# Optimization experiments

Measured on AMD Instinct MI355X. Metric: run time of the kernel, lower is better.

The kernel has to match this reference:

```python
import jax, jax.numpy as jnp
import numpy as np

RELU_NEG_SLOPE = 0.2

def _gat_layer(x, W, a, src, dst, num_nodes, concat):
    # x: [N, Din]; W: [H, Din, F]; a: [H, 2F]; src/dst: [E]
    H, _, F = W.shape
    proj = jnp.einsum('nd,hdf->nhf', x, W)              # [N, H, F]
    a_self, a_nb = a[:, :F], a[:, F:]                   # [H, F] each
    alpha_self = jnp.einsum('nhf,hf->nh', proj, a_self) # [N, H]
    alpha_nb = jnp.einsum('nhf,hf->nh', proj, a_nb)     # [N, H]
    # edge score: a . [proj_dst || proj_src], dst = center node i, src = neighbor j
    e = jax.nn.leaky_relu(alpha_self[dst] + alpha_nb[src], RELU_NEG_SLOPE)  # [E, H]
    e_max = jax.ops.segment_max(e, dst, num_segments=num_nodes)
    e_exp = jnp.exp(e - e_max[dst])
    denom = jax.ops.segment_sum(e_exp, dst, num_segments=num_nodes)
    w = e_exp / denom[dst]                              # [E, H] softmax per dst node
    msg = proj[src] * w[:, :, None]                     # [E, H, F]
    out = jax.ops.segment_sum(msg, dst, num_segments=num_nodes)  # [N, H, F]
    if concat:
        return out.reshape(num_nodes, H * F)
    return out.mean(axis=1)


def setup_inputs() -> dict:
    key = jax.random.key(0)
    k1, k2, k3, k4, k5, k6 = jax.random.split(key, 6)
    N, Din, F1, H1 = 10000, 128, 64, 8
    Dmid = H1 * F1  # 512
    F2, H2 = 64, 1
    x = jax.random.normal(k1, (N, Din), dtype=jnp.float32)
    edges = jax.random.randint(k2, (2, 80000), 0, N, dtype=jnp.int64)
    W1 = jax.random.normal(k3, (H1, Din, F1), dtype=jnp.float32) / np.sqrt(Din)
    a1 = jax.random.normal(k4, (H1, 2 * F1), dtype=jnp.float32) / np.sqrt(2 * F1)
    W2 = jax.random.normal(k5, (H2, Dmid, F2), dtype=jnp.float32) / np.sqrt(Dmid)
    a2 = jax.random.normal(k6, (H2, 2 * F2), dtype=jnp.float32) / np.sqrt(2 * F2)
    return {"x": x, "edges": edges, "W1": W1, "a1": a1, "W2": W2, "a2": a2}


def reference(x, edges, W1, a1, W2, a2):
    N = x.shape[0]
    loops = jnp.arange(N, dtype=edges.dtype)
    # undirected graph + self loops (Graph.neighborhood adds both directions and self)
    src = jnp.concatenate([edges[0], edges[1], loops])
    dst = jnp.concatenate([edges[1], edges[0], loops])
    h = _gat_layer(x, W1, a1, src, dst, N, concat=True)   # [N, 512]
    h = jax.nn.elu(h)
    out = _gat_layer(h, W2, a2, src, dst, N, concat=False)  # [N, 64]
    return out
```

## Files before the change

### kernel.cpp

```cpp
#include <hip/hip_runtime.h>
#include <hip/hip_fp16.h>

#define RELU_NEG_SLOPE 0.2f

typedef _Float16 half8 __attribute__((ext_vector_type(8)));
typedef float f32x4 __attribute__((ext_vector_type(4)));

__device__ __forceinline__ float leaky(float e) {
    return (e > 0.f) ? e : RELU_NEG_SLOPE * e;
}

__device__ __forceinline__ float elu1(float x) {
    return (x > 0.f) ? x : (__expf(x) - 1.f);
}

#define MAXN 16384
#define MAXPAD 16384

__device__ __align__(256) int            g_cnt[MAXN];
__device__ __align__(256) unsigned short g_ell[MAXN * 64];
__device__ __align__(256) __half         g_proj1p[(size_t)4 * MAXPAD * 128];
__device__ __align__(256) __half         g_hbufh[(size_t)MAXPAD * 512];
__device__ __align__(256) __half         g_W2t[64 * 512];
__device__ __align__(256) __half         g_proj2h[MAXN * 64];
__device__ __align__(256) float          g_as1[MAXN * 8];
__device__ __align__(256) float          g_an1[MAXN * 8];
__device__ __align__(256) float          g_as2[MAXN];
__device__ __align__(256) float          g_an2[MAXN];

__global__ __launch_bounds__(256) void k1_scatter_gemm1(
    const int* __restrict__ edges, int E0,
    const float* __restrict__ W2, int t2, int nscat,
    const float4* __restrict__ x4, const float* __restrict__ W1,
    const float* __restrict__ a1, int N, int slabN) {
    __shared__ __half Bs[64 * 132];
    if (blockIdx.x < nscat) {
        int i = blockIdx.x * 256 + threadIdx.x;
        if (i < 2 * E0) {
            int s = edges[i];
            int d = (i < E0) ? edges[E0 + i] : edges[i - E0];
            int pos = atomicAdd(&g_cnt[d], 1);
            g_ell[(d << 6) + pos] = (unsigned short)s;
        } else if (i < 2 * E0 + t2) {
            int j = i - 2 * E0;
            int f = j & 63;
            int d = j >> 6;
            g_W2t[f * 512 + d] = __float2half(W2[j]);
        }
        return;
    }
    int bid2 = blockIdx.x - nscat;
    const int h = bid2 & 7;
    const int by = bid2 >> 3;

    {
        const float4* W1h = (const float4*)W1 + h * 2048;
        int t = threadIdx.x;
#pragma unroll
        for (int r = 0; r < 8; r++) {
            int j4 = t + r * 256;
            float4 w = W1h[j4];
            int f = (j4 << 2) & 63;
            int d = j4 >> 4;
            Bs[(f + 0) * 132 + d] = __float2half(w.x);
            Bs[(f + 1) * 132 + d] = __float2half(w.y);
            Bs[(f + 2) * 132 + d] = __float2half(w.z);
            Bs[(f + 3) * 132 + d] = __float2half(w.w);
        }
    }
    __syncthreads();

    const int lane = threadIdx.x & 63;
    const int wave = threadIdx.x >> 6;
    const int q = lane >> 4;
    const int l15 = lane & 15;
    const int mrow = by * 64 + wave * 16;

    int arow = mrow + l15;
    if (arow >= N) arow = N - 1;
    const float4* Ar = x4 + (size_t)arow * 32;

    f32x4 acc[4] = {{0.f, 0.f, 0.f, 0.f}, {0.f, 0.f, 0.f, 0.f},
                    {0.f, 0.f, 0.f, 0.f}, {0.f, 0.f, 0.f, 0.f}};
#pragma unroll
    for (int ks = 0; ks < 4; ks++) {
        float4 a0 = Ar[ks * 8 + q * 2];
        float4 a1v = Ar[ks * 8 + q * 2 + 1];
        half8 av;
        av[0] = (_Float16)a0.x; av[1] = (_Float16)a0.y;
        av[2] = (_Float16)a0.z; av[3] = (_Float16)a0.w;
        av[4] = (_Float16)a1v.x; av[5] = (_Float16)a1v.y;
        av[6] = (_Float16)a1v.z; av[7] = (_Float16)a1v.w;
#pragma unroll
        for (int t = 0; t < 4; t++) {
            half8 bv = *(const half8*)(Bs + (t * 16 + l15) * 132 + q * 8 + ks * 32);
            acc[t] = __builtin_amdgcn_mfma_f32_16x16x32_f16(av, bv, acc[t], 0, 0, 0);
        }
    }

    __half* Cs = g_proj1p + (size_t)(h >> 1) * slabN + (h & 1) * 64;
    float asc[4], anc[4];
#pragma unroll
    for (int t = 0; t < 4; t++) {
        asc[t] = a1[h * 128 + t * 16 + l15];
        anc[t] = a1[h * 128 + 64 + t * 16 + l15];
    }
#pragma unroll
    for (int r = 0; r < 4; r++) {
        int mg = mrow + q * 4 + r;
        float ps = 0.f, pn = 0.f;
#pragma unroll
        for (int t = 0; t < 4; t++) {
            float v = acc[t][r];
            ps += v * asc[t];
            pn += v * anc[t];
            if (mg < N)
                Cs[(size_t)mg * 128 + t * 16 + l15] = __float2half(v);
        }
#pragma unroll
        for (int m = 8; m >= 1; m >>= 1) {
            ps += __shfl_xor(ps, m, 64);
            pn += __shfl_xor(pn, m, 64);
        }
        if (l15 == 0 && mg < N) {
            g_as1[mg * 8 + h] = ps;
            g_an1[mg * 8 + h] = pn;
        }
    }
}

__global__ __launch_bounds__(256) void agg_h8_sliced(int N, int slabN) {
    int bid = blockIdx.x;
    int hp = bid & 3;
    int rem = bid >> 2;
    int d = rem * 4 + (threadIdx.x >> 6);
    int lane = threadIdx.x & 63;
    if (d >= N) return;
    const int sub = lane >> 3;
    const int inner = lane & 7;
    const int hh = inner >> 2;
    const int h = hp * 2 + hh;
    const int c16 = (inner & 3) * 16;

    int deg = g_cnt[d];
    const unsigned short* row = g_ell + (d << 6);
    float asd = g_as1[d * 8 + h];
    const __half* slab = g_proj1p + (size_t)hp * slabN;

    float acc[16];
#pragma unroll
    for (int i = 0; i < 16; i++) acc[i] = 0.f;
    float den = 0.f;
    if (sub == 0) {
        float e = __expf(leaky(asd + g_an1[d * 8 + h]));
        const __half* p = slab + (size_t)d * 128 + hh * 64 + c16;
        half8 v0 = *(const half8*)p;
        half8 v1 = *(const half8*)(p + 8);
        den = e;
#pragma unroll
        for (int i = 0; i < 8; i++) {
            acc[i] = e * (float)v0[i];
            acc[8 + i] = e * (float)v1[i];
        }
    }
    for (int j0 = 0; j0 < deg; j0 += 16) {
        int ja = j0 + sub;
        int jb = ja + 8;
        int jca = (ja < deg) ? ja : (deg - 1);
        int jcb = (jb < deg) ? jb : (deg - 1);
        int sa = row[jca];
        int sb = row[jcb];
        float na = g_an1[sa * 8 + h];
        float nb = g_an1[sb * 8 + h];
        const __half* pa = slab + (size_t)sa * 128 + hh * 64 + c16;
        const __half* pb = slab + (size_t)sb * 128 + hh * 64 + c16;
        half8 va0 = *(const half8*)pa;
        half8 va1 = *(const half8*)(pa + 8);
        half8 vb0 = *(const half8*)pb;
        half8 vb1 = *(const half8*)(pb + 8);
        float ea = __expf(leaky(asd + na));
        float eb = __expf(leaky(asd + nb));
        if (ja >= deg) ea = 0.f;
        if (jb >= deg) eb = 0.f;
        den += ea + eb;
#pragma unroll
        for (int i = 0; i < 8; i++) {
            acc[i]     += ea * (float)va0[i] + eb * (float)vb0[i];
            acc[8 + i] += ea * (float)va1[i] + eb * (float)vb1[i];
        }
    }

#pragma unroll
    for (int off = 32; off >= 8; off >>= 1) {
#pragma unroll
        for (int i = 0; i < 16; i++) acc[i] += __shfl_down(acc[i], off, 64);
        den += __shfl_down(den, off, 64);
    }

    if (sub == 0) {
        float r = 1.f / den;
        half8 o0, o1;
#pragma unroll
        for (int i = 0; i < 8; i++) {
            o0[i] = (_Float16)elu1(acc[i] * r);
            o1[i] = (_Float16)elu1(acc[8 + i] * r);
        }
        __half* op = g_hbufh + (size_t)d * 512 + h * 64 + c16;
        *(half8*)op = o0;
        *(half8*)(op + 8) = o1;
    }
}

__global__ __launch_bounds__(64) void mfma_gemm2(
    const float* __restrict__ a2, int M) {
    const int lane = threadIdx.x & 63;
    const int q = lane >> 4;
    const int l15 = lane & 15;
    const int mrow = blockIdx.x * 16;

    f32x4 acc[4] = {{0.f, 0.f, 0.f, 0.f}, {0.f, 0.f, 0.f, 0.f},
                    {0.f, 0.f, 0.f, 0.f}, {0.f, 0.f, 0.f, 0.f}};
    const __half* Ap = g_hbufh + (size_t)(mrow + l15) * 512 + q * 8;
    const __half* Bp = g_W2t + (size_t)l15 * 512 + q * 8;
#pragma unroll
    for (int ks = 0; ks < 16; ks++) {
        half8 av = *(const half8*)(Ap + ks * 32);
#pragma unroll
        for (int t = 0; t < 4; t++) {
            half8 bv = *(const half8*)(Bp + (size_t)t * 16 * 512 + ks * 32);
            acc[t] = __builtin_amdgcn_mfma_f32_16x16x32_f16(av, bv, acc[t], 0, 0, 0);
        }
    }

    float asc[4], anc[4];
#pragma unroll
    for (int t = 0; t < 4; t++) {
        asc[t] = a2[t * 16 + l15];
        anc[t] = a2[64 + t * 16 + l15];
    }
#pragma unroll
    for (int r = 0; r < 4; r++) {
        int mg = mrow + q * 4 + r;
        float ps = 0.f, pn = 0.f;
#pragma unroll
        for (int t = 0; t < 4; t++) {
            float v = acc[t][r];
            ps += v * asc[t];
            pn += v * anc[t];
            if (mg < M)
                g_proj2h[(size_t)mg * 64 + t * 16 + l15] = __float2half(v);
        }
#pragma unroll
        for (int m = 8; m >= 1; m >>= 1) {
            ps += __shfl_xor(ps, m, 64);
            pn += __shfl_xor(pn, m, 64);
        }
        if (l15 == 0 && mg < M) {
            g_as2[mg] = ps;
            g_an2[mg] = pn;
        }
    }
}

__global__ __launch_bounds__(256) void agg_node_h1(float* __restrict__ out,
                                                   int N) {
    int d = blockIdx.x * 4 + (threadIdx.x >> 6);
    int lane = threadIdx.x & 63;
    if (d >= N) return;
    int sub = lane >> 3;
    int inner = lane & 7;
    int deg = g_cnt[d];
    if (lane == 0) g_cnt[d] = 0;
    const unsigned short* row = g_ell + (d << 6);
    float asd = g_as2[d];

    float acc[8];
#pragma unroll
    for (int i = 0; i < 8; i++) acc[i] = 0.f;
    float den = 0.f;
    for (int j0 = 0; j0 < deg; j0 += 32) {
        int jj[4], s[4];
        float en[4];
        half8 v[4];
#pragma unroll
        for (int g = 0; g < 4; g++) {
            jj[g] = j0 + g * 8 + sub;
            int jc = (jj[g] < deg) ? jj[g] : (deg - 1);
            s[g] = row[jc];
        }
#pragma unroll
        for (int g = 0; g < 4; g++) en[g] = g_an2[s[g]];
#pragma unroll
        for (int g = 0; g < 4; g++)
            v[g] = *(const half8*)(g_proj2h + (size_t)s[g] * 64 + inner * 8);
#pragma unroll
        for (int g = 0; g < 4; g++) {
            float e = __expf(leaky(asd + en[g]));
            if (jj[g] >= deg) e = 0.f;
            den += e;
#pragma unroll
            for (int i = 0; i < 8; i++) acc[i] += e * (float)v[g][i];
        }
    }

#pragma unroll
    for (int off = 32; off >= 8; off >>= 1) {
#pragma unroll
        for (int i = 0; i < 8; i++) acc[i] += __shfl_down(acc[i], off, 64);
        den += __shfl_down(den, off, 64);
    }

    if (sub == 0) {
        float e = __expf(leaky(asd + g_an2[d]));
        half8 v = *(const half8*)(g_proj2h + (size_t)d * 64 + inner * 8);
        den += e;
#pragma unroll
        for (int i = 0; i < 8; i++) acc[i] += e * (float)v[i];
        float rden = 1.f / den;
        float4 r0, r1;
        r0.x = acc[0] * rden; r0.y = acc[1] * rden;
        r0.z = acc[2] * rden; r0.w = acc[3] * rden;
        r1.x = acc[4] * rden; r1.y = acc[5] * rden;
        r1.z = acc[6] * rden; r1.w = acc[7] * rden;
        float* op = out + (size_t)d * 64 + inner * 8;
        *(float4*)op = r0;
        *(float4*)(op + 4) = r1;
    }
}

extern "C" void kernel_launch(void* const* d_in, const int* in_sizes, int n_in,
                              void* d_out, int out_size, void* d_ws, size_t ws_size,
                              hipStream_t stream) {
    const float* x  = (const float*)d_in[0];
    const int* edges = (const int*)d_in[1];
    const float* W1 = (const float*)d_in[2];
    const float* a1 = (const float*)d_in[3];
    const float* W2 = (const float*)d_in[4];
    const float* a2 = (const float*)d_in[5];

    const int Din = 128, H1 = 8, Dmid = 512;
    const int N = in_sizes[0] / Din;
    const int E0 = in_sizes[1] / 2;
    const int Mpad = (N + 63) & ~63;
    const int slabN = Mpad * 128;
    (void)d_ws; (void)ws_size;

    int t2 = Dmid * 64;
    int nscat = (2 * E0 + t2 + 255) / 256;
    int ngemm = H1 * (Mpad / 64);
    k1_scatter_gemm1<<<nscat + ngemm, 256, 0, stream>>>(
        edges, E0, W2, t2, nscat, (const float4*)x, W1, a1, N, slabN);

    int nbp = (N + 3) / 4;
    agg_h8_sliced<<<4 * nbp, 256, 0, stream>>>(N, slabN);

    mfma_gemm2<<<(N + 15) / 16, 64, 0, stream>>>(a2, N);

    agg_node_h1<<<(N + 3) / 4, 256, 0, stream>>>((float*)d_out, N);
}
```

Measured before the change: 131.5 us.

## Compute two heads per GEMM1 block and unroll aggregation gather by four

Each GEMM1 block now handles a pair of heads, staging both W1 slices in shared memory. This halves the number of GEMM blocks and reuses each loaded and converted x tile across two heads' MFMAs. Separately, the layer-1 aggregation loop processes 32 neighbours per iteration in four groups, issuing all index, score and feature loads before the arithmetic to expose more memory-level parallelism. The cost is double the LDS and accumulator registers in GEMM1, higher register pressure in the aggregation kernel, and fewer GEMM blocks for parallelism.

```diff
diff --git a/kernel.cpp b/kernel.cpp
--- a/kernel.cpp
+++ b/kernel.cpp
@@ -33,7 +33,7 @@
     const float* __restrict__ W2, int t2, int nscat,
     const float4* __restrict__ x4, const float* __restrict__ W1,
     const float* __restrict__ a1, int N, int slabN) {
-    __shared__ __half Bs[64 * 132];
+    __shared__ __half Bs[2][64 * 132];
     if (blockIdx.x < nscat) {
         int i = blockIdx.x * 256 + threadIdx.x;
         if (i < 2 * E0) {
@@ -50,11 +50,12 @@
         return;
     }
     int bid2 = blockIdx.x - nscat;
-    const int h = bid2 & 7;
-    const int by = bid2 >> 3;
-
-    {
-        const float4* W1h = (const float4*)W1 + h * 2048;
+    const int hp = bid2 & 3;
+    const int by = bid2 >> 2;
+
+#pragma unroll
+    for (int hh = 0; hh < 2; hh++) {
+        const float4* W1h = (const float4*)W1 + (hp * 2 + hh) * 2048;
         int t = threadIdx.x;
 #pragma unroll
         for (int r = 0; r < 8; r++) {
@@ -62,10 +63,10 @@
             float4 w = W1h[j4];
             int f = (j4 << 2) & 63;
             int d = j4 >> 4;
-            Bs[(f + 0) * 132 + d] = __float2half(w.x);
-            Bs[(f + 1) * 132 + d] = __float2half(w.y);
-            Bs[(f + 2) * 132 + d] = __float2half(w.z);
-            Bs[(f + 3) * 132 + d] = __float2half(w.w);
+            Bs[hh][(f + 0) * 132 + d] = __float2half(w.x);
+            Bs[hh][(f + 1) * 132 + d] = __float2half(w.y);
+            Bs[hh][(f + 2) * 132 + d] = __float2half(w.z);
+            Bs[hh][(f + 3) * 132 + d] = __float2half(w.w);
         }
     }
     __syncthreads();
@@ -80,8 +81,11 @@
     if (arow >= N) arow = N - 1;
     const float4* Ar = x4 + (size_t)arow * 32;
 
-    f32x4 acc[4] = {{0.f, 0.f, 0.f, 0.f}, {0.f, 0.f, 0.f, 0.f},
-                    {0.f, 0.f, 0.f, 0.f}, {0.f, 0.f, 0.f, 0.f}};
+    f32x4 acc[2][4];
+#pragma unroll
+    for (int hh = 0; hh < 2; hh++)
+#pragma unroll
+        for (int t = 0; t < 4; t++) acc[hh][t] = {0.f, 0.f, 0.f, 0.f};
 #pragma unroll
     for (int ks = 0; ks < 4; ks++) {
         float4 a0 = Ar[ks * 8 + q * 2];
@@ -92,39 +96,46 @@
         av[4] = (_Float16)a1v.x; av[5] = (_Float16)a1v.y;
         av[6] = (_Float16)a1v.z; av[7] = (_Float16)a1v.w;
 #pragma unroll
+        for (int hh = 0; hh < 2; hh++) {
+#pragma unroll
+            for (int t = 0; t < 4; t++) {
+                half8 bv = *(const half8*)(&Bs[hh][(t * 16 + l15) * 132 + q * 8 + ks * 32]);
+                acc[hh][t] = __builtin_amdgcn_mfma_f32_16x16x32_f16(av, bv, acc[hh][t], 0, 0, 0);
+            }
+        }
+    }
+
+#pragma unroll
+    for (int hh = 0; hh < 2; hh++) {
+        const int h = hp * 2 + hh;
+        __half* Cs = g_proj1p + (size_t)hp * slabN + hh * 64;
+        float asc[4], anc[4];
+#pragma unroll
         for (int t = 0; t < 4; t++) {
-            half8 bv = *(const half8*)(Bs + (t * 16 + l15) * 132 + q * 8 + ks * 32);
-            acc[t] = __builtin_amdgcn_mfma_f32_16x16x32_f16(av, bv, acc[t], 0, 0, 0);
-        }
-    }
-
-    __half* Cs = g_proj1p + (size_t)(h >> 1) * slabN + (h & 1) * 64;
-    float asc[4], anc[4];
-#pragma unroll
-    for (int t = 0; t < 4; t++) {
-        asc[t] = a1[h * 128 + t * 16 + l15];
-        anc[t] = a1[h * 128 + 64 + t * 16 + l15];
-    }
-#pragma unroll
-    for (int r = 0; r < 4; r++) {
-        int mg = mrow + q * 4 + r;
-        float ps = 0.f, pn = 0.f;
-#pragma unroll
-        for (int t = 0; t < 4; t++) {
-            float v = acc[t][r];
-            ps += v * asc[t];
-            pn += v * anc[t];
-            if (mg < N)
-                Cs[(size_t)mg * 128 + t * 16 + l15] = __float2half(v);
-        }
-#pragma unroll
-        for (int m = 8; m >= 1; m >>= 1) {
-            ps += __shfl_xor(ps, m, 64);
-            pn += __shfl_xor(pn, m, 64);
-        }
-        if (l15 == 0 && mg < N) {
-            g_as1[mg * 8 + h] = ps;
-            g_an1[mg * 8 + h] = pn;
+            asc[t] = a1[h * 128 + t * 16 + l15];
+            anc[t] = a1[h * 128 + 64 + t * 16 + l15];
+        }
+#pragma unroll
+        for (int r = 0; r < 4; r++) {
+            int mg = mrow + q * 4 + r;
+            float ps = 0.f, pn = 0.f;
+#pragma unroll
+            for (int t = 0; t < 4; t++) {
+                float v = acc[hh][t][r];
+                ps += v * asc[t];
+                pn += v * anc[t];
+                if (mg < N)
+                    Cs[(size_t)mg * 128 + t * 16 + l15] = __float2half(v);
+            }
+#pragma unroll
+            for (int m = 8; m >= 1; m >>= 1) {
+                ps += __shfl_xor(ps, m, 64);
+                pn += __shfl_xor(pn, m, 64);
+            }
+            if (l15 == 0 && mg < N) {
+                g_as1[mg * 8 + h] = ps;
+                g_an1[mg * 8 + h] = pn;
+            }
         }
     }
 }
@@ -163,30 +174,34 @@
             acc[8 + i] = e * (float)v1[i];
         }
     }
-    for (int j0 = 0; j0 < deg; j0 += 16) {
-        int ja = j0 + sub;
-        int jb = ja + 8;
-        int jca = (ja < deg) ? ja : (deg - 1);
-        int jcb = (jb < deg) ? jb : (deg - 1);
-        int sa = row[jca];
-        int sb = row[jcb];
-        float na = g_an1[sa * 8 + h];
-        float nb = g_an1[sb * 8 + h];
-        const __half* pa = slab + (size_t)sa * 128 + hh * 64 + c16;
-        const __half* pb = slab + (size_t)sb * 128 + hh * 64 + c16;
-        half8 va0 = *(const half8*)pa;
-        half8 va1 = *(const half8*)(pa + 8);
-        half8 vb0 = *(const half8*)pb;
-        half8 vb1 = *(const half8*)(pb + 8);
-        float ea = __expf(leaky(asd + na));
-        float eb = __expf(leaky(asd + nb));
-        if (ja >= deg) ea = 0.f;
-        if (jb >= deg) eb = 0.f;
-        den += ea + eb;
-#pragma unroll
-        for (int i = 0; i < 8; i++) {
-            acc[i]     += ea * (float)va0[i] + eb * (float)vb0[i];
-            acc[8 + i] += ea * (float)va1[i] + eb * (float)vb1[i];
+    for (int j0 = 0; j0 < deg; j0 += 32) {
+        int jj[4], sv[4];
+        float en[4];
+        half8 v0[4], v1[4];
+#pragma unroll
+        for (int g = 0; g < 4; g++) {
+            jj[g] = j0 + g * 8 + sub;
+            int jc = (jj[g] < deg) ? jj[g] : (deg - 1);
+            sv[g] = row[jc];
+        }
+#pragma unroll
+        for (int g = 0; g < 4; g++) en[g] = g_an1[sv[g] * 8 + h];
+#pragma unroll
+        for (int g = 0; g < 4; g++) {
+            const __half* p = slab + (size_t)sv[g] * 128 + hh * 64 + c16;
+            v0[g] = *(const half8*)p;
+            v1[g] = *(const half8*)(p + 8);
+        }
+#pragma unroll
+        for (int g = 0; g < 4; g++) {
+            float e = __expf(leaky(asd + en[g]));
+            if (jj[g] >= deg) e = 0.f;
+            den += e;
+#pragma unroll
+            for (int i = 0; i < 8; i++) {
+                acc[i]     += e * (float)v0[g][i];
+                acc[8 + i] += e * (float)v1[g][i];
+            }
         }
     }
 
@@ -338,16 +353,16 @@
     const float* W2 = (const float*)d_in[4];
     const float* a2 = (const float*)d_in[5];
 
-    const int Din = 128, H1 = 8, Dmid = 512;
+    const int Din = 128, Dmid = 512;
     const int N = in_sizes[0] / Din;
     const int E0 = in_sizes[1] / 2;
     const int Mpad = (N + 63) & ~63;
     const int slabN = Mpad * 128;
-    (void)d_ws; (void)ws_size;
+    (void)W1; (void)d_ws; (void)ws_size;
 
     int t2 = Dmid * 64;
     int nscat = (2 * E0 + t2 + 255) / 256;
-    int ngemm = H1 * (Mpad / 64);
+    int ngemm = 4 * (Mpad / 64);
     k1_scatter_gemm1<<<nscat + ngemm, 256, 0, stream>>>(
         edges, E0, W2, t2, nscat, (const float4*)x, W1, a1, N, slabN);
 
```

Measured after the change: 138.4 us. 5.2% more time.
